# Performance work log

Hardware: AMD Instinct MI355X
Metric: run time of the kernel (lower is better)

## Reference

```python
import jax, jax.numpy as jnp
import numpy as np

N, C, L, K = 8, 128, 1024, 100   # batch, channels, encoded seq len, num_negatives
TEMP = 0.5                        # contrastive temperature
EPS = 1e-8                        # cosine-similarity norm clamp (torch default)


def setup_inputs() -> dict:
    key = jax.random.key(0)
    kz, kc, kn = jax.random.split(key, 3)
    z = jax.random.normal(kz, (N, C, L), dtype=jnp.float32)
    c = jax.random.normal(kc, (N, C, L + 1), dtype=jnp.float32)
    # Uniform sampling of K distinct indices per (n, l), excluding l itself:
    # equivalent to torch.multinomial(ones(L,L)-eye(L), K) per row, per sample.
    noise = jax.random.uniform(kn, (N, L, L), dtype=jnp.float32)
    noise = noise - 2.0 * jnp.eye(L, dtype=jnp.float32)  # push self-index below everything
    _, neg_inds = jax.lax.top_k(noise, K)                # (N, L, K) int32, distinct, != l
    return {"z": z, "c": c, "neg_inds": neg_inds.astype(jnp.int32)}


def reference(z, c, neg_inds):
    # z: (N, C, L) unmasked convencoder features; c: (N, C, L+1) transformer out
    n, ch, l = z.shape
    z_seq = jnp.transpose(z, (0, 2, 1))                  # (N, L, C)
    # gather negatives: (N, L, K, C)
    negatives = z_seq[jnp.arange(n)[:, None, None], neg_inds]
    # drop start token, move to (N, L, 1, C)
    c_seq = jnp.transpose(c[..., 1:], (0, 2, 1))[:, :, None, :]
    z_tgt = z_seq[:, :, None, :]                         # (N, L, 1, C)
    targets = jnp.concatenate([z_tgt, negatives], axis=2)  # (N, L, K+1, C)
    # cosine similarity along C with torch-style eps clamping
    dot = jnp.sum(c_seq * targets, axis=-1)              # (N, L, K+1)
    c_norm = jnp.maximum(jnp.sqrt(jnp.sum(c_seq * c_seq, axis=-1)), EPS)
    t_norm = jnp.maximum(jnp.sqrt(jnp.sum(targets * targets, axis=-1)), EPS)
    logits = dot / (c_norm * t_norm) / TEMP              # (N, L, K+1)
    # mask negatives that exactly equal the context vector
    neg_in_tgt = jnp.all(c_seq == negatives, axis=-1)    # (N, L, K)
    neg_logits = jnp.where(neg_in_tgt, -jnp.inf, logits[:, :, 1:])
    logits = jnp.concatenate([logits[:, :, :1], neg_logits], axis=2)
    return logits.reshape(-1, K + 1)                     # (N*L, K+1)
```

## Files before the change

### kernel.cpp

```cpp
#include <hip/hip_runtime.h>
#include <math.h>

#define N 8
#define C 128
#define L 1024
#define K 100
#define TEMP 0.5f
#define EPS 1e-8f
#define NT (N * L)

typedef _Float16 h2 __attribute__((ext_vector_type(2)));
union U4 { uint4 u; h2 h[4]; };

__device__ __forceinline__ float fd2(h2 a, h2 b, float acc) {
#if __has_builtin(__builtin_amdgcn_fdot2)
    return __builtin_amdgcn_fdot2(a, b, acc, false);
#else
    return acc + (float)a[0] * (float)b[0] + (float)a[1] * (float)b[1];
#endif
}

#if __has_builtin(__builtin_amdgcn_mov_dpp)
#define DPP_ADD(x, ctrl) ((x) + __int_as_float(__builtin_amdgcn_mov_dpp(__float_as_int(x), (ctrl), 0xF, 0xF, true)))
#else
#define DPP_ADD(x, ctrl) ((x) + __shfl_xor((x), ((ctrl) == 0xB1 ? 1 : 2)))
#endif

__global__ void __launch_bounds__(512)
transpose_both(const float* __restrict__ z, const float* __restrict__ c,
               _Float16* __restrict__ z_h, _Float16* __restrict__ c_h,
               float* __restrict__ zp, float* __restrict__ cp) {
    __shared__ float tile[64][65];
    __shared__ float part[8][64];
    const int which = blockIdx.z >> 3;
    const int n = blockIdx.z & 7;
    const float* src = which ? c : z;
    _Float16* dst = which ? c_h : z_h;
    float* pdst = which ? cp : zp;
    const int slen = which ? (L + 1) : L;
    const int off = which;
    const int l0 = blockIdx.x * 64;
    const int c0 = blockIdx.y * 64;
    const int tx = threadIdx.x;
    const int ty = threadIdx.y;
#pragma unroll
    for (int i = 0; i < 8; i++) {
        int chn = c0 + ty + i * 8;
        tile[ty + i * 8][tx] = src[((size_t)(n * C + chn)) * slen + off + l0 + tx];
    }
    __syncthreads();
#pragma unroll
    for (int i = 0; i < 8; i++) {
        int l = l0 + ty + i * 8;
        dst[((size_t)n * L + l) * C + c0 + tx] = (_Float16)tile[tx][ty + i * 8];
    }
    float p = 0.f;
#pragma unroll
    for (int i = 0; i < 8; i++) { float v = tile[ty * 8 + i][tx]; p += v * v; }
    part[ty][tx] = p;
    __syncthreads();
    if (ty == 0) {
        float sm = 0.f;
#pragma unroll
        for (int i = 0; i < 8; i++) sm += part[i][tx];
        pdst[(((size_t)n << 10) + l0 + tx) * 2 + (c0 >> 6)] = sm;
    }
}

__global__ void __launch_bounds__(256)
ssl_main(const _Float16* __restrict__ zh, const _Float16* __restrict__ chh,
         const int* __restrict__ neg_inds,
         const float* __restrict__ zp, const float* __restrict__ cp,
         const float* __restrict__ z_orig, const float* __restrict__ c_orig,
         float* __restrict__ out) {
    const int tid  = threadIdx.x;
    const int lane = tid & 63;
    const int g    = lane >> 2;
    const int s    = lane & 3;
    const int nt   = blockIdx.x * 4 + (tid >> 6);
    const int n    = nt >> 10;
    const int t    = nt & (L - 1);

    const uint4* crow = (const uint4*)(chh + (size_t)nt * C);
    U4 cf[4];
#pragma unroll
    for (int j = 0; j < 4; j++) cf[j].u = crow[s + 4 * j];

    const float2 cpv = ((const float2*)cp)[nt];
    const float cn = cpv.x + cpv.y;
    const float rs_c = 2.0f * rsqrtf(fmaxf(cn, EPS * EPS));

    const int* ni = neg_inds + (size_t)nt * K;
    const _Float16* zbase = zh + (((size_t)n) << 10) * C;
    const float2* zp2 = (const float2*)zp + ((size_t)n << 10);

    int idxs[7];
#pragma unroll
    for (int i = 0; i < 7; i++) {
        int kk = i * 16 + g;
        idxs[i] = (kk == 0) ? t : ((kk <= K) ? ni[kk - 1] : 0);
    }
    float tns[7];
#pragma unroll
    for (int i = 0; i < 7; i++) { float2 tv = zp2[idxs[i]]; tns[i] = tv.x + tv.y; }

    U4 rows[7][4];
#pragma unroll
    for (int p = 0; p < 2; p++) {
        const uint4* zr = (const uint4*)(zbase + (size_t)idxs[p] * C);
#pragma unroll
        for (int j = 0; j < 4; j++) rows[p][j].u = zr[s + 4 * j];
    }

#pragma unroll
    for (int i = 0; i < 7; i++) {
        if (i + 2 < 7) {
            const uint4* zr = (const uint4*)(zbase + (size_t)idxs[i + 2] * C);
#pragma unroll
            for (int j = 0; j < 4; j++) rows[i + 2][j].u = zr[s + 4 * j];
        }

        float d0 = 0.f, d1 = 0.f;
#pragma unroll
        for (int j = 0; j < 4; j++) {
            d0 = fd2(cf[j].h[0], rows[i][j].h[0], d0);
            d1 = fd2(cf[j].h[1], rows[i][j].h[1], d1);
            d0 = fd2(cf[j].h[2], rows[i][j].h[2], d0);
            d1 = fd2(cf[j].h[3], rows[i][j].h[3], d1);
        }
        float dot = d0 + d1;
        dot = DPP_ADD(dot, 0xB1);
        dot = DPP_ADD(dot, 0x4E);

        int kk = i * 16 + g;
        if (s == 0 && kk <= K) {
            float logit = dot * rs_c * rsqrtf(fmaxf(tns[i], EPS * EPS));
            if (kk > 0) {
                float ds = cn - 2.f * dot + tns[i];
                if (ds < 0.05f * cn) {
                    bool eq = true;
                    for (int q = 0; q < C; q++) {
                        float cv = c_orig[((size_t)(n * C + q)) * (L + 1) + t + 1];
                        float zv = z_orig[((size_t)(n * C + q)) * L + idxs[i]];
                        eq = eq && (cv == zv);
                    }
                    if (eq) logit = -INFINITY;
                }
            }
            out[(size_t)nt * (K + 1) + kk] = logit;
        }
    }
}

extern "C" void kernel_launch(void* const* d_in, const int* in_sizes, int n_in,
                              void* d_out, int out_size, void* d_ws, size_t ws_size,
                              hipStream_t stream) {
    const float* z   = (const float*)d_in[0];
    const float* c   = (const float*)d_in[1];
    const int*   neg = (const int*)d_in[2];
    float* out = (float*)d_out;

    _Float16* z_h = (_Float16*)d_ws;
    _Float16* c_h = z_h + (size_t)NT * C;
    float* zp = (float*)(c_h + (size_t)NT * C);
    float* cp = zp + (size_t)NT * 2;

    transpose_both<<<dim3(L / 64, C / 64, 16), dim3(64, 8), 0, stream>>>(z, c, z_h, c_h, zp, cp);
    ssl_main<<<dim3(NT / 4), 256, 0, stream>>>(z_h, c_h, neg, zp, cp, z, c, out);
}
```

Measured before the change: 79.79 us.

## Stage z tiles in swizzled LDS and gather negatives per tile via ballot lists

The main kernel is restructured so each block loads a 256-row quarter of z (fp16) into XOR-swizzled shared memory along with 32 context rows. Each negative index is then routed to the block owning its quarter, with ballot/mbcnt compaction building per-row hit lists. Dot products read z rows from LDS instead of doing random global gathers. The cost is that every neg_inds row is read by four blocks, and the LDS footprint is large, which limits occupancy.

```diff
diff --git a/kernel.cpp b/kernel.cpp
--- a/kernel.cpp
+++ b/kernel.cpp
@@ -9,8 +9,12 @@
 #define EPS 1e-8f
 #define NT (N * L)
 
+#define TQ 256
+#define TT 32
+#define HCAP 104
+
 typedef _Float16 h2 __attribute__((ext_vector_type(2)));
-union U4 { uint4 u; h2 h[4]; };
+typedef _Float16 v8h __attribute__((ext_vector_type(8)));
 
 __device__ __forceinline__ float fd2(h2 a, h2 b, float acc) {
 #if __has_builtin(__builtin_amdgcn_fdot2)
@@ -41,8 +45,7 @@
     const int off = which;
     const int l0 = blockIdx.x * 64;
     const int c0 = blockIdx.y * 64;
-    const int tx = threadIdx.x;
-    const int ty = threadIdx.y;
+    const int tx = threadIdx.x, ty = threadIdx.y;
 #pragma unroll
     for (int i = 0; i < 8; i++) {
         int chn = c0 + ty + i * 8;
@@ -67,87 +70,119 @@
     }
 }
 
-__global__ void __launch_bounds__(256)
-ssl_main(const _Float16* __restrict__ zh, const _Float16* __restrict__ chh,
-         const int* __restrict__ neg_inds,
-         const float* __restrict__ zp, const float* __restrict__ cp,
-         const float* __restrict__ z_orig, const float* __restrict__ c_orig,
-         float* __restrict__ out) {
-    const int tid  = threadIdx.x;
-    const int lane = tid & 63;
-    const int g    = lane >> 2;
-    const int s    = lane & 3;
-    const int nt   = blockIdx.x * 4 + (tid >> 6);
-    const int n    = nt >> 10;
-    const int t    = nt & (L - 1);
-
-    const uint4* crow = (const uint4*)(chh + (size_t)nt * C);
-    U4 cf[4];
-#pragma unroll
-    for (int j = 0; j < 4; j++) cf[j].u = crow[s + 4 * j];
-
-    const float2 cpv = ((const float2*)cp)[nt];
-    const float cn = cpv.x + cpv.y;
-    const float rs_c = 2.0f * rsqrtf(fmaxf(cn, EPS * EPS));
-
-    const int* ni = neg_inds + (size_t)nt * K;
-    const _Float16* zbase = zh + (((size_t)n) << 10) * C;
-    const float2* zp2 = (const float2*)zp + ((size_t)n << 10);
-
-    int idxs[7];
-#pragma unroll
-    for (int i = 0; i < 7; i++) {
-        int kk = i * 16 + g;
-        idxs[i] = (kk == 0) ? t : ((kk <= K) ? ni[kk - 1] : 0);
-    }
-    float tns[7];
-#pragma unroll
-    for (int i = 0; i < 7; i++) { float2 tv = zp2[idxs[i]]; tns[i] = tv.x + tv.y; }
-
-    U4 rows[7][4];
-#pragma unroll
-    for (int p = 0; p < 2; p++) {
-        const uint4* zr = (const uint4*)(zbase + (size_t)idxs[p] * C);
-#pragma unroll
-        for (int j = 0; j < 4; j++) rows[p][j].u = zr[s + 4 * j];
-    }
-
-#pragma unroll
-    for (int i = 0; i < 7; i++) {
-        if (i + 2 < 7) {
-            const uint4* zr = (const uint4*)(zbase + (size_t)idxs[i + 2] * C);
-#pragma unroll
-            for (int j = 0; j < 4; j++) rows[i + 2][j].u = zr[s + 4 * j];
+__global__ void __launch_bounds__(256, 2)
+lds_gather(const _Float16* __restrict__ zh, const _Float16* __restrict__ chh,
+           const int* __restrict__ neg,
+           const float* __restrict__ zp, const float* __restrict__ cp,
+           const float* __restrict__ z_orig, const float* __restrict__ c_orig,
+           float* __restrict__ out) {
+    __shared__ __align__(16) _Float16 zl[TQ * C];
+    __shared__ __align__(16) _Float16 cl[TT * C];
+    __shared__ float zn[TQ];
+    __shared__ float cns[TT];
+    __shared__ unsigned short hits[4][8][HCAP];
+    __shared__ int nh_sh[4][8];
+
+    const int tid = threadIdx.x;
+    const int q  = blockIdx.x;
+    const int tc = blockIdx.y;
+    const int n  = blockIdx.z;
+    const int w = tid >> 6, lane = tid & 63;
+    const int g = lane >> 2, s = lane & 3;
+
+    {
+        const uint4* src = (const uint4*)(zh + ((size_t)(n * L + q * TQ)) * C);
+#pragma unroll
+        for (int i = 0; i < 16; i++) {
+            int flat = i * 256 + tid;
+            int row = flat >> 4, chk = flat & 15;
+            uint4 v = src[flat];
+            *(uint4*)(zl + row * C + (((chk ^ (row & 15)) << 3))) = v;
         }
-
-        float d0 = 0.f, d1 = 0.f;
-#pragma unroll
-        for (int j = 0; j < 4; j++) {
-            d0 = fd2(cf[j].h[0], rows[i][j].h[0], d0);
-            d1 = fd2(cf[j].h[1], rows[i][j].h[1], d1);
-            d0 = fd2(cf[j].h[2], rows[i][j].h[2], d0);
-            d1 = fd2(cf[j].h[3], rows[i][j].h[3], d1);
+    }
+    {
+        const uint4* src = (const uint4*)(chh + ((size_t)(n * L + tc * TT)) * C);
+        uint4* dst = (uint4*)cl;
+        dst[tid] = src[tid];
+        dst[tid + 256] = src[tid + 256];
+    }
+    {
+        const float2* zp2 = (const float2*)zp + (size_t)n * L + q * TQ;
+        float2 v = zp2[tid];
+        zn[tid] = v.x + v.y;
+        if (tid < TT) {
+            float2 u = ((const float2*)cp)[(size_t)n * L + tc * TT + tid];
+            cns[tid] = u.x + u.y;
         }
-        float dot = d0 + d1;
-        dot = DPP_ADD(dot, 0xB1);
-        dot = DPP_ADD(dot, 0x4E);
-
-        int kk = i * 16 + g;
-        if (s == 0 && kk <= K) {
-            float logit = dot * rs_c * rsqrtf(fmaxf(tns[i], EPS * EPS));
-            if (kk > 0) {
-                float ds = cn - 2.f * dot + tns[i];
-                if (ds < 0.05f * cn) {
-                    bool eq = true;
-                    for (int q = 0; q < C; q++) {
-                        float cv = c_orig[((size_t)(n * C + q)) * (L + 1) + t + 1];
-                        float zv = z_orig[((size_t)(n * C + q)) * L + idxs[i]];
-                        eq = eq && (cv == zv);
+    }
+    for (int i = 0; i < 8; i++) {
+        int tt = w * 8 + i;
+        int tg = tc * TT + tt;
+        const int* ni = neg + ((size_t)n * L + tg) * K;
+        int ia = (lane == 0) ? tg : ni[lane - 1];
+        bool pa = (ia >> 8) == q;
+        int ib = (lane < K - 63) ? ni[63 + lane] : -1;
+        bool pb = (lane < K - 63) && ((ib >> 8) == q);
+        unsigned long long ba = __ballot(pa);
+        unsigned long long bb = __ballot(pb);
+        int posa = __builtin_amdgcn_mbcnt_hi((unsigned)(ba >> 32),
+                   __builtin_amdgcn_mbcnt_lo((unsigned)ba, 0));
+        int ca = __popcll(ba);
+        int posb = ca + __builtin_amdgcn_mbcnt_hi((unsigned)(bb >> 32),
+                   __builtin_amdgcn_mbcnt_lo((unsigned)bb, 0));
+        if (pa) hits[w][i][posa] = (unsigned short)((lane << 8) | (ia & 255));
+        if (pb) hits[w][i][posb] = (unsigned short)(((64 + lane) << 8) | (ib & 255));
+        if (lane == 0) nh_sh[w][i] = ca + __popcll(bb);
+    }
+    __syncthreads();
+
+    for (int i = 0; i < 8; i++) {
+        const int tt = w * 8 + i;
+        const int tg = tc * TT + tt;
+        const size_t nt = (size_t)n * L + tg;
+        v8h cf[4];
+#pragma unroll
+        for (int j = 0; j < 4; j++)
+            cf[j] = *(const v8h*)(cl + tt * C + ((s + 4 * j) << 3));
+        const float cn = cns[tt];
+        const float rcn = rsqrtf(fmaxf(cn, EPS * EPS));
+        const int nh = nh_sh[w][i];
+        const unsigned short* hl = hits[w][i];
+        float* orow = out + nt * (K + 1);
+        for (int h0 = 0; h0 < nh; h0 += 16) {
+            int slot = h0 + g;
+            if (slot < nh) {
+                int e = hl[slot];
+                int kk = e >> 8, il = e & 255, key = il & 15;
+                const _Float16* zr = zl + il * C;
+                float d0 = 0.f, d1 = 0.f;
+#pragma unroll
+                for (int j = 0; j < 4; j++) {
+                    v8h zv = *(const v8h*)(zr + (((s + 4 * j) ^ key) << 3));
+                    const h2* cz = (const h2*)&cf[j];
+                    const h2* zz = (const h2*)&zv;
+                    d0 = fd2(cz[0], zz[0], d0);
+                    d1 = fd2(cz[1], zz[1], d1);
+                    d0 = fd2(cz[2], zz[2], d0);
+                    d1 = fd2(cz[3], zz[3], d1);
+                }
+                float dot = d0 + d1;
+                dot = DPP_ADD(dot, 0xB1);
+                dot = DPP_ADD(dot, 0x4E);
+                if (s == 0) {
+                    float tn = zn[il];
+                    float logit = 2.0f * dot * rcn * rsqrtf(fmaxf(tn, EPS * EPS));
+                    if (kk > 0 && (cn - 2.f * dot + tn) < 0.05f * cn) {
+                        int idx = (q << 8) | il;
+                        bool eq = true;
+                        for (int p = 0; p < C; p++)
+                            eq = eq && (c_orig[((size_t)(n * C + p)) * (L + 1) + tg + 1] ==
+                                        z_orig[((size_t)(n * C + p)) * L + idx]);
+                        if (eq) logit = -INFINITY;
                     }
-                    if (eq) logit = -INFINITY;
+                    orow[kk] = logit;
                 }
             }
-            out[(size_t)nt * (K + 1) + kk] = logit;
         }
     }
 }
@@ -166,5 +201,5 @@
     float* cp = zp + (size_t)NT * 2;
 
     transpose_both<<<dim3(L / 64, C / 64, 16), dim3(64, 8), 0, stream>>>(z, c, z_h, c_h, zp, cp);
-    ssl_main<<<dim3(NT / 4), 256, 0, stream>>>(z_h, c_h, neg, zp, cp, z, c, out);
-}
+    lds_gather<<<dim3(4, L / TT, N), 256, 0, stream>>>(z_h, c_h, neg, zp, cp, z, c, out);
+}
```

After: 92.12 us. 1.15x slower.

## Pre-normalize rows in transpose and split each query across two waves

Applied to the files above, without the earlier changes.

The transpose kernel now handles all 128 channels per 32-position chunk, computes each row's norm, and stores pre-scaled fp16 rows. The context rows also carry the 1/TEMP factor, so the dot product is the logit directly. This removes the separate norm buffers and the per-logit rsqrt math in the main kernel. The main kernel gives each query position two waves, each covering about half of the 101 targets, which raises parallelism and cuts the unrolled row registers from 7 to 4. The cheap equality pre-filter becomes a threshold on the normalized logit. Normalizing before the fp16 cast slightly changes rounding.

```diff
diff --git a/kernel.cpp b/kernel.cpp
--- a/kernel.cpp
+++ b/kernel.cpp
@@ -10,7 +10,7 @@
 #define NT (N * L)
 
 typedef _Float16 h2 __attribute__((ext_vector_type(2)));
-union U4 { uint4 u; h2 h[4]; };
+typedef _Float16 v8h __attribute__((ext_vector_type(8)));
 
 __device__ __forceinline__ float fd2(h2 a, h2 b, float acc) {
 #if __has_builtin(__builtin_amdgcn_fdot2)
@@ -26,126 +26,119 @@
 #define DPP_ADD(x, ctrl) ((x) + __shfl_xor((x), ((ctrl) == 0xB1 ? 1 : 2)))
 #endif
 
-__global__ void __launch_bounds__(512)
-transpose_both(const float* __restrict__ z, const float* __restrict__ c,
-               _Float16* __restrict__ z_h, _Float16* __restrict__ c_h,
-               float* __restrict__ zp, float* __restrict__ cp) {
-    __shared__ float tile[64][65];
-    __shared__ float part[8][64];
-    const int which = blockIdx.z >> 3;
-    const int n = blockIdx.z & 7;
+__global__ void __launch_bounds__(256)
+norm_transpose(const float* __restrict__ z, const float* __restrict__ c,
+               _Float16* __restrict__ z_h, _Float16* __restrict__ c_h) {
+    __shared__ float tile[C][33];
+    __shared__ float part[8][32];
+    __shared__ float scale_s[32];
+    const int chunk = blockIdx.x;
+    const int which = blockIdx.y;
+    const int n = blockIdx.z;
     const float* src = which ? c : z;
     _Float16* dst = which ? c_h : z_h;
-    float* pdst = which ? cp : zp;
     const int slen = which ? (L + 1) : L;
     const int off = which;
-    const int l0 = blockIdx.x * 64;
-    const int c0 = blockIdx.y * 64;
-    const int tx = threadIdx.x;
-    const int ty = threadIdx.y;
+    const int tid = threadIdx.x;
+    const int tx = tid & 31;
+    const int ty = tid >> 5;
+
 #pragma unroll
-    for (int i = 0; i < 8; i++) {
-        int chn = c0 + ty + i * 8;
-        tile[ty + i * 8][tx] = src[((size_t)(n * C + chn)) * slen + off + l0 + tx];
+    for (int i = 0; i < 16; i++) {
+        int ch = ty + 8 * i;
+        tile[ch][tx] = src[((size_t)(n * C + ch)) * slen + off + chunk * 32 + tx];
     }
     __syncthreads();
+    float sm = 0.f;
 #pragma unroll
-    for (int i = 0; i < 8; i++) {
-        int l = l0 + ty + i * 8;
-        dst[((size_t)n * L + l) * C + c0 + tx] = (_Float16)tile[tx][ty + i * 8];
-    }
-    float p = 0.f;
-#pragma unroll
-    for (int i = 0; i < 8; i++) { float v = tile[ty * 8 + i][tx]; p += v * v; }
-    part[ty][tx] = p;
+    for (int i = 0; i < 16; i++) { float v = tile[ty * 16 + i][tx]; sm += v * v; }
+    part[ty][tx] = sm;
     __syncthreads();
     if (ty == 0) {
-        float sm = 0.f;
+        float s2 = 0.f;
 #pragma unroll
-        for (int i = 0; i < 8; i++) sm += part[i][tx];
-        pdst[(((size_t)n << 10) + l0 + tx) * 2 + (c0 >> 6)] = sm;
+        for (int i = 0; i < 8; i++) s2 += part[i][tx];
+        float nrm = fmaxf(sqrtf(s2), EPS);
+        scale_s[tx] = (which ? 2.0f : 1.0f) / nrm;
+    }
+    __syncthreads();
+    const int ch = tid & 127;
+    const int lq = tid >> 7;
+#pragma unroll
+    for (int j = 0; j < 16; j++) {
+        int l = lq + 2 * j;
+        dst[((size_t)(n * L + chunk * 32 + l)) * C + ch] =
+            (_Float16)(tile[ch][l] * scale_s[l]);
     }
 }
 
 __global__ void __launch_bounds__(256)
-ssl_main(const _Float16* __restrict__ zh, const _Float16* __restrict__ chh,
-         const int* __restrict__ neg_inds,
-         const float* __restrict__ zp, const float* __restrict__ cp,
-         const float* __restrict__ z_orig, const float* __restrict__ c_orig,
-         float* __restrict__ out) {
+ssl2(const _Float16* __restrict__ zh, const _Float16* __restrict__ chh,
+     const int* __restrict__ neg,
+     const float* __restrict__ z_orig, const float* __restrict__ c_orig,
+     float* __restrict__ out) {
     const int tid  = threadIdx.x;
     const int lane = tid & 63;
     const int g    = lane >> 2;
     const int s    = lane & 3;
-    const int nt   = blockIdx.x * 4 + (tid >> 6);
+    const int h    = (tid >> 6) & 1;
+    const int nt   = blockIdx.x * 2 + (tid >> 7);
     const int n    = nt >> 10;
     const int t    = nt & (L - 1);
 
-    const uint4* crow = (const uint4*)(chh + (size_t)nt * C);
-    U4 cf[4];
+    const v8h* crow = (const v8h*)(chh + (size_t)nt * C);
+    v8h cf[4];
 #pragma unroll
-    for (int j = 0; j < 4; j++) cf[j].u = crow[s + 4 * j];
+    for (int j = 0; j < 4; j++) cf[j] = crow[s + 4 * j];
 
-    const float2 cpv = ((const float2*)cp)[nt];
-    const float cn = cpv.x + cpv.y;
-    const float rs_c = 2.0f * rsqrtf(fmaxf(cn, EPS * EPS));
+    const int* ni = neg + (size_t)nt * K;
+    const _Float16* zbase = zh + (((size_t)n) << 10) * C;
+    const int base = h * 51;
+    const int kmax = h ? 101 : 51;
 
-    const int* ni = neg_inds + (size_t)nt * K;
-    const _Float16* zbase = zh + (((size_t)n) << 10) * C;
-    const float2* zp2 = (const float2*)zp + ((size_t)n << 10);
-
-    int idxs[7];
+    int idxs[4];
 #pragma unroll
-    for (int i = 0; i < 7; i++) {
-        int kk = i * 16 + g;
-        idxs[i] = (kk == 0) ? t : ((kk <= K) ? ni[kk - 1] : 0);
-    }
-    float tns[7];
-#pragma unroll
-    for (int i = 0; i < 7; i++) { float2 tv = zp2[idxs[i]]; tns[i] = tv.x + tv.y; }
-
-    U4 rows[7][4];
-#pragma unroll
-    for (int p = 0; p < 2; p++) {
-        const uint4* zr = (const uint4*)(zbase + (size_t)idxs[p] * C);
-#pragma unroll
-        for (int j = 0; j < 4; j++) rows[p][j].u = zr[s + 4 * j];
+    for (int i = 0; i < 4; i++) {
+        int kk = base + i * 16 + g;
+        idxs[i] = (kk == 0) ? t : ((kk < kmax) ? ni[kk - 1] : 0);
     }
 
+    v8h rows[4][4];
+    {
+        const v8h* zr = (const v8h*)(zbase + (size_t)idxs[0] * C);
 #pragma unroll
-    for (int i = 0; i < 7; i++) {
-        if (i + 2 < 7) {
-            const uint4* zr = (const uint4*)(zbase + (size_t)idxs[i + 2] * C);
+        for (int j = 0; j < 4; j++) rows[0][j] = zr[s + 4 * j];
+    }
 #pragma unroll
-            for (int j = 0; j < 4; j++) rows[i + 2][j].u = zr[s + 4 * j];
+    for (int i = 0; i < 4; i++) {
+        if (i + 1 < 4) {
+            const v8h* zr = (const v8h*)(zbase + (size_t)idxs[i + 1] * C);
+#pragma unroll
+            for (int j = 0; j < 4; j++) rows[i + 1][j] = zr[s + 4 * j];
         }
-
         float d0 = 0.f, d1 = 0.f;
 #pragma unroll
         for (int j = 0; j < 4; j++) {
-            d0 = fd2(cf[j].h[0], rows[i][j].h[0], d0);
-            d1 = fd2(cf[j].h[1], rows[i][j].h[1], d1);
-            d0 = fd2(cf[j].h[2], rows[i][j].h[2], d0);
-            d1 = fd2(cf[j].h[3], rows[i][j].h[3], d1);
+            const h2* cz = (const h2*)&cf[j];
+            const h2* zz = (const h2*)&rows[i][j];
+            d0 = fd2(cz[0], zz[0], d0);
+            d1 = fd2(cz[1], zz[1], d1);
+            d0 = fd2(cz[2], zz[2], d0);
+            d1 = fd2(cz[3], zz[3], d1);
         }
         float dot = d0 + d1;
         dot = DPP_ADD(dot, 0xB1);
         dot = DPP_ADD(dot, 0x4E);
 
-        int kk = i * 16 + g;
-        if (s == 0 && kk <= K) {
-            float logit = dot * rs_c * rsqrtf(fmaxf(tns[i], EPS * EPS));
-            if (kk > 0) {
-                float ds = cn - 2.f * dot + tns[i];
-                if (ds < 0.05f * cn) {
-                    bool eq = true;
-                    for (int q = 0; q < C; q++) {
-                        float cv = c_orig[((size_t)(n * C + q)) * (L + 1) + t + 1];
-                        float zv = z_orig[((size_t)(n * C + q)) * L + idxs[i]];
-                        eq = eq && (cv == zv);
-                    }
-                    if (eq) logit = -INFINITY;
-                }
+        int kk = base + i * 16 + g;
+        if (s == 0 && kk < kmax) {
+            float logit = dot;
+            if (kk > 0 && dot > 1.9f) {
+                bool eq = true;
+                for (int q = 0; q < C; q++)
+                    eq = eq && (c_orig[((size_t)(n * C + q)) * (L + 1) + t + 1] ==
+                                z_orig[((size_t)(n * C + q)) * L + idxs[i]]);
+                if (eq) logit = -INFINITY;
             }
             out[(size_t)nt * (K + 1) + kk] = logit;
         }
@@ -162,9 +155,7 @@
 
     _Float16* z_h = (_Float16*)d_ws;
     _Float16* c_h = z_h + (size_t)NT * C;
-    float* zp = (float*)(c_h + (size_t)NT * C);
-    float* cp = zp + (size_t)NT * 2;
 
-    transpose_both<<<dim3(L / 64, C / 64, 16), dim3(64, 8), 0, stream>>>(z, c, z_h, c_h, zp, cp);
-    ssl_main<<<dim3(NT / 4), 256, 0, stream>>>(z_h, c_h, neg, zp, cp, z, c, out);
+    norm_transpose<<<dim3(32, 2, N), 256, 0, stream>>>(z, c, z_h, c_h);
+    ssl2<<<dim3(NT / 2), 256, 0, stream>>>(z_h, c_h, neg, z, c, out);
 }
```

Measured after the change: 81.30 us. About the same (+1.9%).
